# Kernel optimization log

Measured on AMD Instinct MI355X. Metric: run time of the kernel, lower is better.

Reference implementation:

```python
import jax, jax.numpy as jnp
import numpy as np

B, S, D, H = 8, 1024, 512, 12
HS = D // H  # 42 (head_size; 12*42 = 504 concat width, as in the original)


def setup_inputs() -> dict:
    key = jax.random.key(0)
    ks = jax.random.split(key, 12)
    sd = 0.02
    return {
        "embedded_patches": jax.random.normal(ks[0], (B, S, D), dtype=jnp.float32),
        # stacked per-head projections (12 independent Linear(D, HS, bias=False))
        "wk": jax.random.normal(ks[1], (H, D, HS), dtype=jnp.float32) * sd,
        "wq": jax.random.normal(ks[2], (H, D, HS), dtype=jnp.float32) * sd,
        "wv": jax.random.normal(ks[3], (H, D, HS), dtype=jnp.float32) * sd,
        "w_proj": jax.random.normal(ks[4], (H * HS, D), dtype=jnp.float32) * sd,  # [504, 512]
        "b_proj": jnp.zeros((D,), dtype=jnp.float32),
        # shared LayerNorm (same params used for both norms, as in the original)
        "gamma": jnp.ones((D,), dtype=jnp.float32),
        "beta": jnp.zeros((D,), dtype=jnp.float32),
        "w1": jax.random.normal(ks[5], (D, 4 * D), dtype=jnp.float32) * sd,
        "b1": jnp.zeros((4 * D,), dtype=jnp.float32),
        "w2": jax.random.normal(ks[6], (4 * D, D), dtype=jnp.float32) * sd,
        "b2": jnp.zeros((D,), dtype=jnp.float32),
    }


def _layernorm(x, gamma, beta, eps=1e-5):
    mu = jnp.mean(x, axis=-1, keepdims=True)
    var = jnp.var(x, axis=-1, keepdims=True)
    return (x - mu) * jax.lax.rsqrt(var + eps) * gamma + beta


def reference(embedded_patches, wk, wq, wv, w_proj, b_proj, gamma, beta, w1, b1, w2, b2):
    x = embedded_patches
    n1 = _layernorm(x, gamma, beta)
    # per-head projections, vectorized over heads: [B,S,D] x [H,D,E] -> [B,H,S,E]
    q = jnp.einsum('bsd,hde->bhse', n1, wq)
    k = jnp.einsum('bsd,hde->bhse', n1, wk)
    v = jnp.einsum('bsd,hde->bhse', n1, wv)
    scale = HS ** -0.5
    wei = jax.nn.softmax(jnp.einsum('bhse,bhte->bhst', q, k) * scale, axis=-1)
    out = jnp.einsum('bhst,bhte->bhse', wei, v)        # [B,H,S,E]
    out = out.transpose(0, 2, 1, 3).reshape(B, S, H * HS)  # concat heads -> [B,S,504]
    attn = out @ w_proj + b_proj                       # [B,S,D]
    # original quirk: takes batch element 0 and broadcasts against residual
    first_added = attn[0] + x                          # [S,D] + [B,S,D] -> [B,S,D]
    n2 = _layernorm(first_added, gamma, beta)
    h = jax.nn.gelu(n2 @ w1 + b1, approximate=False)   # torch nn.GELU default = exact erf
    ff = h @ w2 + b2
    return ff + first_added
```

## Files before the change

kernel.cpp:

```cpp
#include <hip/hip_runtime.h>
#include <hip/hip_bf16.h>
#include <stdint.h>


typedef unsigned short u16;
typedef __attribute__((ext_vector_type(8))) short short8;
typedef __attribute__((ext_vector_type(4))) float f32x4;

__device__ __forceinline__ u16 f2bf(float f) {
  union { float f; unsigned u; } x; x.f = f;
  return (u16)((x.u + 0x7FFFu + ((x.u >> 16) & 1u)) >> 16);
}
__device__ __forceinline__ float bf2f(u16 u) {
  union { unsigned u; float f; } x; x.u = ((unsigned)u) << 16;
  return x.f;
}

__device__ __forceinline__ void gload_lds16(const u16* g, u16* l) {
  __builtin_amdgcn_global_load_lds(
      (__attribute__((address_space(1))) void*)g,
      (__attribute__((address_space(3))) void*)l, 16, 0, 0);
}

__device__ __forceinline__ float wred_sum(float v) {
#pragma unroll
  for (int off = 32; off > 0; off >>= 1) v += __shfl_xor(v, off, 64);
  return v;
}
__device__ __forceinline__ float wred_max(float v) {
#pragma unroll
  for (int off = 32; off > 0; off >>= 1) v = fmaxf(v, __shfl_xor(v, off, 64));
  return v;
}

__device__ __forceinline__ float gelu_fast(float t) {
  const float p = __builtin_fmaf(0.0356774081f, t * t, 0.7978845608f);
  return t / (1.0f + __expf(-2.0f * t * p));
}

#define MFMA16x16(a, b, c) __builtin_amdgcn_mfma_f32_16x16x32_bf16(a, b, c, 0, 0, 0)

enum { EP_BF16 = 0, EP_F32B = 2, EP_GELU = 3, EP_PVPART = 6, EP_ATOM = 7 };

template <int EP>
__launch_bounds__(256, 4)
__global__ void gemm2(const u16* __restrict__ A, int lda, long sAz,
                      const u16* __restrict__ Bt, int ldb, long sBz,
                      void* __restrict__ Cv, int ldc, long sCz,
                      int K, const float* __restrict__ bias,
                      const float* __restrict__ aux) {
  __shared__ u16 lA[2][128 * 32];
  __shared__ u16 lB[2][128 * 32];

  const int gx = gridDim.x, gy = gridDim.y;
  const int lin = blockIdx.x + gx * (blockIdx.y + gy * blockIdx.z);
  const int nwg = gx * gy * gridDim.z;
  const int wg = (lin & 7) * (nwg >> 3) + (lin >> 3);
  const int bx = wg % gx;
  const int tmp = wg / gx;
  const int by = tmp % gy;
  const int z = tmp / gy;

  const u16* Ab;
  const u16* Bb;
  if (EP == EP_PVPART) {
    Ab = A + (long)(z >> 2) * sAz + (z & 3) * 256;
    Bb = Bt + (long)(z >> 2) * sBz + (z & 3) * 256;
  } else {
    Ab = A + (long)z * sAz;
    Bb = Bt + (long)z * sBz;
  }
  const int m0 = bx * 128;
  const int n0 = by * 128;
  const int tid = threadIdx.x;
  const int w = tid >> 6;
  const int l = tid & 63;
  const int wr = w >> 1;
  const int wc = w & 1;
  const int NT = K >> 5;

  f32x4 acc[4][4];
#pragma unroll
  for (int i = 0; i < 4; ++i)
#pragma unroll
    for (int j = 0; j < 4; ++j) acc[i][j] = (f32x4){0.f, 0.f, 0.f, 0.f};

  const int srow = w * 32 + (l >> 2);
  const int sk = (l & 3) * 8;
  const u16* ga0 = Ab + (long)(m0 + srow) * lda + sk;
  const u16* ga1 = Ab + (long)(m0 + srow + 16) * lda + sk;
  const u16* gb0 = Bb + (long)(n0 + srow) * ldb + sk;
  const u16* gb1 = Bb + (long)(n0 + srow + 16) * ldb + sk;
  const int dOff = w * 1024;

  const int aoff = (wr * 64 + (l & 15)) * 32 + (l >> 4) * 8;
  const int boff = (wc * 64 + (l & 15)) * 32 + (l >> 4) * 8;

  gload_lds16(ga0, &lA[0][dOff]);
  gload_lds16(ga1, &lA[0][dOff + 512]);
  gload_lds16(gb0, &lB[0][dOff]);
  gload_lds16(gb1, &lB[0][dOff + 512]);
  __syncthreads();

  int buf = 0;
  for (int t = 0; t < NT; ++t) {
    short8 af[4], bfv[4];
#pragma unroll
    for (int mi = 0; mi < 4; ++mi)
      af[mi] = *(const short8*)&lA[buf][aoff + mi * 16 * 32];
#pragma unroll
    for (int ni = 0; ni < 4; ++ni)
      bfv[ni] = *(const short8*)&lB[buf][boff + ni * 16 * 32];
    if (t + 1 < NT) {
      const int k0 = (t + 1) * 32;
      const int nb = buf ^ 1;
      gload_lds16(ga0 + k0, &lA[nb][dOff]);
      gload_lds16(ga1 + k0, &lA[nb][dOff + 512]);
      gload_lds16(gb0 + k0, &lB[nb][dOff]);
      gload_lds16(gb1 + k0, &lB[nb][dOff + 512]);
    }
#pragma unroll
    for (int mi = 0; mi < 4; ++mi)
#pragma unroll
      for (int ni = 0; ni < 4; ++ni)
        acc[mi][ni] = MFMA16x16(af[mi], bfv[ni], acc[mi][ni]);
    __syncthreads();
    buf ^= 1;
  }

  const int rbase = m0 + wr * 64 + (l >> 4) * 4;
  const int cbase = n0 + wc * 64 + (l & 15);
#pragma unroll
  for (int mi = 0; mi < 4; ++mi) {
#pragma unroll
    for (int ni = 0; ni < 4; ++ni) {
#pragma unroll
      for (int j = 0; j < 4; ++j) {
        const int row = rbase + mi * 16 + j;
        const int col = cbase + ni * 16;
        const float v = acc[mi][ni][j];
        if (EP == EP_BF16) {
          ((u16*)Cv)[(long)z * sCz + (long)row * ldc + col] = f2bf(v);
        } else if (EP == EP_F32B) {
          ((float*)Cv)[(long)row * ldc + col] = v + bias[col];
        } else if (EP == EP_GELU) {
          ((u16*)Cv)[(long)row * ldc + col] = f2bf(gelu_fast(v + bias[col]));
        } else if (EP == EP_PVPART) {
          ((float*)Cv)[(long)z * sCz + (long)row * ldc + col] = v;
        } else {
          atomicAdd(&((float*)Cv)[(long)row * ldc + col], v);
        }
      }
    }
  }
}

__global__ void combine_pv_kernel(const float* __restrict__ part,
                                  const float* __restrict__ invl,
                                  u16* __restrict__ cat) {
  const int i = blockIdx.x * 256 + threadIdx.x;
  const int e = i % 42;
  const int rowh = i / 42;
  const int row = rowh & 1023;
  const int h = rowh >> 10;
  const long base = (long)(h * 4) * 131072 + row * 128 + e;
  float v = part[base] + part[base + 131072] + part[base + 2 * 131072] +
            part[base + 3 * 131072];
  cat[(long)row * 512 + h * 42 + e] = f2bf(v * invl[h * 1024 + row]);
}

__device__ __forceinline__ void transpose_body(const float* __restrict__ in,
                                               u16* __restrict__ out, int N,
                                               int Kin, int Kpad, int blk,
                                               int gx, int t, float* smem) {
  const int n0 = (blk % gx) * 64;
  const int k0 = (blk / gx) * 64;
  const int tc = t & 63;
  const int tr = t >> 6;
#pragma unroll
  for (int r = 0; r < 16; ++r) {
    const int kr = tr * 16 + r;
    const int kg = k0 + kr;
    smem[kr * 65 + tc] = (kg < Kin) ? in[(long)kg * N + n0 + tc] : 0.f;
  }
  __syncthreads();
  const int nr0 = t >> 4;
  const int kc = (t & 15) * 4;
#pragma unroll
  for (int p = 0; p < 4; ++p) {
    const int nr = nr0 + p * 16;
    ushort4 v;
    v.x = f2bf(smem[(kc + 0) * 65 + nr]);
    v.y = f2bf(smem[(kc + 1) * 65 + nr]);
    v.z = f2bf(smem[(kc + 2) * 65 + nr]);
    v.w = f2bf(smem[(kc + 3) * 65 + nr]);
    *(ushort4*)&out[(long)(n0 + nr) * Kpad + k0 + kc] = v;
  }
}

__global__ void prep_fused(const float* __restrict__ wq,
                           const float* __restrict__ wk,
                           const float* __restrict__ wv,
                           const float* __restrict__ w_proj,
                           const float* __restrict__ w1,
                           const float* __restrict__ w2,
                           const float* __restrict__ x,
                           const float* __restrict__ gamma,
                           const float* __restrict__ beta,
                           u16* __restrict__ BtQKV, u16* __restrict__ wvT,
                           u16* __restrict__ BtP, u16* __restrict__ Bt1,
                           u16* __restrict__ Bt2, u16* __restrict__ cat,
                           u16* __restrict__ n1, float scale) {
  __shared__ float smem[64 * 65];
  const int blk = blockIdx.x;
  const int t = threadIdx.x;
  if (blk < 3072) {
    const int i = blk * 256 + t;
    const int n = i >> 9, d = i & 511;
    const int pq = n / 768;
    const int h = (n % 768) >> 6;
    const int e = n & 63;
    float v = 0.f;
    if (e < 42) {
      v = (pq ? wk : wq)[((long)h * 512 + d) * 42 + e];
      if (!pq) v *= scale;
    }
    BtQKV[i] = f2bf(v);
  } else if (blk < 6144) {
    const int i = (blk - 3072) * 256 + t;
    const int r = i >> 9, d = i & 511;
    const int h = r >> 7, e = r & 127;
    wvT[i] = f2bf(e < 42 ? wv[((long)h * 512 + d) * 42 + e] : 0.f);
  } else if (blk < 6208) {
    transpose_body(w_proj, BtP, 512, 504, 512, blk - 6144, 8, t, smem);
  } else if (blk < 6464) {
    transpose_body(w1, Bt1, 2048, 512, 512, blk - 6208, 32, t, smem);
  } else if (blk < 6720) {
    transpose_body(w2, Bt2, 512, 2048, 2048, blk - 6464, 8, t, smem);
  } else if (blk < 8768) {
    cat[(blk - 6720) * 256 + t] = 0;
  } else {
    const int s = blk - 8768;
    const float* row = x + (long)s * 512;
    const float v0 = row[t];
    const float v1 = row[t + 256];
    float sum = wred_sum(v0 + v1);
    float sq = wred_sum(v0 * v0 + v1 * v1);
    if ((t & 63) == 0) { smem[t >> 6] = sum; smem[8 + (t >> 6)] = sq; }
    __syncthreads();
    sum = smem[0] + smem[1] + smem[2] + smem[3];
    sq = smem[8] + smem[9] + smem[10] + smem[11];
    const float mu = sum * (1.0f / 512.0f);
    const float rstd = rsqrtf(sq * (1.0f / 512.0f) - mu * mu + 1e-5f);
    n1[(long)s * 512 + t] = f2bf((v0 - mu) * rstd * gamma[t] + beta[t]);
    n1[(long)s * 512 + t + 256] =
        f2bf((v1 - mu) * rstd * gamma[t + 256] + beta[t + 256]);
  }
}

__global__ void ln2_kernel(const float* __restrict__ x,
                           const float* __restrict__ aproj,
                           const float* __restrict__ gamma,
                           const float* __restrict__ beta,
                           const float* __restrict__ b2,
                           float* __restrict__ fa, u16* __restrict__ n2,
                           float* __restrict__ outp) {
  __shared__ float red[16];
  const int r = blockIdx.x;
  const int t = threadIdx.x;
  const int s = r & 1023;
  const float* xr = x + (long)r * 512;
  const float* ar = aproj + (long)s * 512;
  const float v0 = xr[t] + ar[t];
  const float v1 = xr[t + 256] + ar[t + 256];
  fa[(long)r * 512 + t] = v0;
  fa[(long)r * 512 + t + 256] = v1;
  outp[(long)r * 512 + t] = v0 + b2[t];
  outp[(long)r * 512 + t + 256] = v1 + b2[t + 256];
  float sum = wred_sum(v0 + v1);
  float sq = wred_sum(v0 * v0 + v1 * v1);
  if ((t & 63) == 0) { red[t >> 6] = sum; red[8 + (t >> 6)] = sq; }
  __syncthreads();
  sum = red[0] + red[1] + red[2] + red[3];
  sq = red[8] + red[9] + red[10] + red[11];
  const float mu = sum * (1.0f / 512.0f);
  const float rstd = rsqrtf(sq * (1.0f / 512.0f) - mu * mu + 1e-5f);
  n2[(long)r * 512 + t] = f2bf((v0 - mu) * rstd * gamma[t] + beta[t]);
  n2[(long)r * 512 + t + 256] =
      f2bf((v1 - mu) * rstd * gamma[t + 256] + beta[t + 256]);
}

__global__ void softmax_kernel(u16* __restrict__ SP, float* __restrict__ invl) {
  __shared__ float red[16];
  const long row = blockIdx.x;
  u16* p = SP + row * 1024;
  const int t = threadIdx.x;
  uint2 u = ((const uint2*)p)[t];
  const float s0 = bf2f((u16)(u.x & 0xffff));
  const float s1 = bf2f((u16)(u.x >> 16));
  const float s2 = bf2f((u16)(u.y & 0xffff));
  const float s3 = bf2f((u16)(u.y >> 16));
  float m = wred_max(fmaxf(fmaxf(s0, s1), fmaxf(s2, s3)));
  if ((t & 63) == 0) red[t >> 6] = m;
  __syncthreads();
  m = fmaxf(fmaxf(red[0], red[1]), fmaxf(red[2], red[3]));
  const float e0 = __expf(s0 - m), e1 = __expf(s1 - m);
  const float e2 = __expf(s2 - m), e3 = __expf(s3 - m);
  float sum = wred_sum(e0 + e1 + e2 + e3);
  if ((t & 63) == 0) red[8 + (t >> 6)] = sum;
  __syncthreads();
  sum = red[8] + red[9] + red[10] + red[11];
  if (t == 0) invl[row] = 1.0f / sum;
  uint2 o;
  o.x = (unsigned)f2bf(e0) | ((unsigned)f2bf(e1) << 16);
  o.y = (unsigned)f2bf(e2) | ((unsigned)f2bf(e3) << 16);
  ((uint2*)p)[t] = o;
}

extern "C" void kernel_launch(void* const* d_in, const int* in_sizes, int n_in,
                              void* d_out, int out_size, void* d_ws,
                              size_t ws_size, hipStream_t stream) {
  const float* x = (const float*)d_in[0];
  const float* wk = (const float*)d_in[1];
  const float* wq = (const float*)d_in[2];
  const float* wv = (const float*)d_in[3];
  const float* w_proj = (const float*)d_in[4];
  const float* b_proj = (const float*)d_in[5];
  const float* gamma = (const float*)d_in[6];
  const float* beta = (const float*)d_in[7];
  const float* w1 = (const float*)d_in[8];
  const float* b1 = (const float*)d_in[9];
  const float* w2 = (const float*)d_in[10];
  const float* b2 = (const float*)d_in[11];

  char* base = (char*)d_ws;
  size_t off = 0;
  auto alloc = [&](size_t bytes) -> void* {
    void* p = base + off;
    off += (bytes + 255) & ~(size_t)255;
    return p;
  };
  u16* n1 = (u16*)alloc(1024L * 512 * 2);
  u16* qkvc = (u16*)alloc(1024L * 1536 * 2);
  u16* SP = (u16*)alloc(12L * 1024 * 1024 * 2);
  u16* wvT = (u16*)alloc(1536L * 512 * 2);
  u16* vt = (u16*)alloc(1536L * 1024 * 2);
  u16* cat = (u16*)alloc(1024L * 512 * 2);
  float* aproj = (float*)alloc(1024L * 512 * 4);
  float* fa = (float*)alloc(8192L * 512 * 4);
  u16* n2 = (u16*)alloc(8192L * 512 * 2);
  u16* hbuf = (u16*)alloc(8192L * 2048 * 2);
  u16* BtQKV = (u16*)alloc(1536L * 512 * 2);
  u16* BtP = (u16*)alloc(512L * 512 * 2);
  u16* Bt1 = (u16*)alloc(2048L * 512 * 2);
  u16* Bt2 = (u16*)alloc(512L * 2048 * 2);
  float* invl = (float*)alloc(12L * 1024 * 4);
  float* pvpart = (float*)alloc(48L * 1024 * 128 * 4);
  (void)ws_size; (void)in_sizes; (void)n_in; (void)out_size;

  const float scale = 0.15430334996209191f;

  prep_fused<<<9792, 256, 0, stream>>>(wq, wk, wv, w_proj, w1, w2, x, gamma,
                                       beta, BtQKV, wvT, BtP, Bt1, Bt2, cat,
                                       n1, scale);

  gemm2<EP_BF16><<<dim3(8, 12, 1), 256, 0, stream>>>(
      n1, 512, 0, BtQKV, 512, 0, qkvc, 1536, 0, 512, nullptr, nullptr);
  gemm2<EP_BF16><<<dim3(12, 8, 1), 256, 0, stream>>>(
      wvT, 512, 0, n1, 512, 0, vt, 1024, 0, 512, nullptr, nullptr);
  gemm2<EP_BF16><<<dim3(8, 8, 12), 256, 0, stream>>>(
      qkvc, 1536, 64, qkvc + 768, 1536, 64, SP, 1024, 1024L * 1024, 64,
      nullptr, nullptr);
  softmax_kernel<<<12288, 256, 0, stream>>>(SP, invl);
  gemm2<EP_PVPART><<<dim3(8, 1, 48), 256, 0, stream>>>(
      SP, 1024, 1024L * 1024, vt, 1024, 128L * 1024, pvpart, 128,
      1024L * 128, 256, nullptr, nullptr);
  combine_pv_kernel<<<2016, 256, 0, stream>>>(pvpart, invl, cat);
  gemm2<EP_F32B><<<dim3(8, 4, 1), 256, 0, stream>>>(
      cat, 512, 0, BtP, 512, 0, aproj, 512, 0, 512, b_proj, nullptr);
  ln2_kernel<<<8192, 256, 0, stream>>>(x, aproj, gamma, beta, b2, fa, n2,
                                       (float*)d_out);
  gemm2<EP_GELU><<<dim3(64, 16, 1), 256, 0, stream>>>(
      n2, 512, 0, Bt1, 512, 0, hbuf, 2048, 0, 512, b1, nullptr);
  gemm2<EP_ATOM><<<dim3(64, 4, 2), 256, 0, stream>>>(
      hbuf, 2048, 1024, Bt2, 2048, 1024, d_out, 512, 0, 1024, nullptr,
      nullptr);
}
```

Measured before the change: 177.0 us.

## Fuse attention QK, softmax and PV into a single flash-attention kernel

```diff
diff --git a/kernel.cpp b/kernel.cpp
--- a/kernel.cpp
+++ b/kernel.cpp
@@ -27,11 +27,6 @@
   for (int off = 32; off > 0; off >>= 1) v += __shfl_xor(v, off, 64);
   return v;
 }
-__device__ __forceinline__ float wred_max(float v) {
-#pragma unroll
-  for (int off = 32; off > 0; off >>= 1) v = fmaxf(v, __shfl_xor(v, off, 64));
-  return v;
-}
 
 __device__ __forceinline__ float gelu_fast(float t) {
   const float p = __builtin_fmaf(0.0356774081f, t * t, 0.7978845608f);
@@ -40,15 +35,14 @@
 
 #define MFMA16x16(a, b, c) __builtin_amdgcn_mfma_f32_16x16x32_bf16(a, b, c, 0, 0, 0)
 
-enum { EP_BF16 = 0, EP_F32B = 2, EP_GELU = 3, EP_PVPART = 6, EP_ATOM = 7 };
+enum { EP_BF16 = 0, EP_F32B = 2, EP_GELU = 3, EP_ATOM = 7 };
 
 template <int EP>
 __launch_bounds__(256, 4)
 __global__ void gemm2(const u16* __restrict__ A, int lda, long sAz,
                       const u16* __restrict__ Bt, int ldb, long sBz,
                       void* __restrict__ Cv, int ldc, long sCz,
-                      int K, const float* __restrict__ bias,
-                      const float* __restrict__ aux) {
+                      int K, const float* __restrict__ bias) {
   __shared__ u16 lA[2][128 * 32];
   __shared__ u16 lB[2][128 * 32];
 
@@ -61,15 +55,8 @@
   const int by = tmp % gy;
   const int z = tmp / gy;
 
-  const u16* Ab;
-  const u16* Bb;
-  if (EP == EP_PVPART) {
-    Ab = A + (long)(z >> 2) * sAz + (z & 3) * 256;
-    Bb = Bt + (long)(z >> 2) * sBz + (z & 3) * 256;
-  } else {
-    Ab = A + (long)z * sAz;
-    Bb = Bt + (long)z * sBz;
-  }
+  const u16* Ab = A + (long)z * sAz;
+  const u16* Bb = Bt + (long)z * sBz;
   const int m0 = bx * 128;
   const int n0 = by * 128;
   const int tid = threadIdx.x;
@@ -145,8 +132,6 @@
           ((float*)Cv)[(long)row * ldc + col] = v + bias[col];
         } else if (EP == EP_GELU) {
           ((u16*)Cv)[(long)row * ldc + col] = f2bf(gelu_fast(v + bias[col]));
-        } else if (EP == EP_PVPART) {
-          ((float*)Cv)[(long)z * sCz + (long)row * ldc + col] = v;
         } else {
           atomicAdd(&((float*)Cv)[(long)row * ldc + col], v);
         }
@@ -155,18 +140,133 @@
   }
 }
 
-__global__ void combine_pv_kernel(const float* __restrict__ part,
-                                  const float* __restrict__ invl,
-                                  u16* __restrict__ cat) {
-  const int i = blockIdx.x * 256 + threadIdx.x;
-  const int e = i % 42;
-  const int rowh = i / 42;
-  const int row = rowh & 1023;
-  const int h = rowh >> 10;
-  const long base = (long)(h * 4) * 131072 + row * 128 + e;
-  float v = part[base] + part[base + 131072] + part[base + 2 * 131072] +
-            part[base + 3 * 131072];
-  cat[(long)row * 512 + h * 42 + e] = f2bf(v * invl[h * 1024 + row]);
+__device__ __forceinline__ short8 frag_read(const u16* base, int row, int ks,
+                                            int l) {
+  const int g = (ks * 4 + (l >> 4)) ^ (l & 7);
+  return *(const short8*)&base[row * 64 + g * 8];
+}
+
+__launch_bounds__(256, 2)
+__global__ void flash_attn(const u16* __restrict__ qkvc,
+                           const u16* __restrict__ vt,
+                           u16* __restrict__ cat) {
+  __shared__ u16 lQ[64 * 64];
+  __shared__ u16 lK[2][64 * 64];
+  __shared__ u16 lV[2][64 * 64];
+  __shared__ u16 lP[4][16 * 64];
+  const int h = blockIdx.x;
+  const int q0 = blockIdx.y * 64;
+  const int tid = threadIdx.x;
+  const int w = tid >> 6;
+  const int l = tid & 63;
+  const int sg = ((l & 7) ^ (l >> 3)) * 8;
+  const int sr = w * 8 + (l >> 3);
+
+#define FA_STAGE(t_, b_)                                                    \
+  do {                                                                      \
+    const int kv_ = (t_) * 64;                                              \
+    gload_lds16(qkvc + (long)(kv_ + sr) * 1536 + 768 + h * 64 + sg,         \
+                lK[b_] + w * 8 * 64);                                       \
+    gload_lds16(qkvc + (long)(kv_ + 32 + sr) * 1536 + 768 + h * 64 + sg,    \
+                lK[b_] + (32 + w * 8) * 64);                                \
+    gload_lds16(vt + (long)(h * 128 + sr) * 1024 + kv_ + sg,                \
+                lV[b_] + w * 8 * 64);                                       \
+    gload_lds16(vt + (long)(h * 128 + 32 + sr) * 1024 + kv_ + sg,           \
+                lV[b_] + (32 + w * 8) * 64);                                \
+  } while (0)
+
+  gload_lds16(qkvc + (long)(q0 + sr) * 1536 + h * 64 + sg, lQ + w * 8 * 64);
+  gload_lds16(qkvc + (long)(q0 + 32 + sr) * 1536 + h * 64 + sg,
+              lQ + (32 + w * 8) * 64);
+  FA_STAGE(0, 0);
+  __syncthreads();
+
+  const short8 qf0 = frag_read(lQ, w * 16 + (l & 15), 0, l);
+  const short8 qf1 = frag_read(lQ, w * 16 + (l & 15), 1, l);
+
+  f32x4 accO[4];
+  float m_run[4], l_run[4];
+#pragma unroll
+  for (int i = 0; i < 4; ++i) {
+    accO[i] = (f32x4){0.f, 0.f, 0.f, 0.f};
+    m_run[i] = -3.0e38f;
+    l_run[i] = 0.f;
+  }
+
+  int buf = 0;
+  for (int t = 0; t < 16; ++t) {
+    if (t + 1 < 16) FA_STAGE(t + 1, buf ^ 1);
+    f32x4 s[4];
+#pragma unroll
+    for (int ni = 0; ni < 4; ++ni) {
+      const short8 kf0 = frag_read(lK[buf], ni * 16 + (l & 15), 0, l);
+      const short8 kf1 = frag_read(lK[buf], ni * 16 + (l & 15), 1, l);
+      s[ni] = MFMA16x16(qf0, kf0, ((f32x4){0.f, 0.f, 0.f, 0.f}));
+      s[ni] = MFMA16x16(qf1, kf1, s[ni]);
+    }
+#pragma unroll
+    for (int j = 0; j < 4; ++j) {
+      float mx = fmaxf(fmaxf(s[0][j], s[1][j]), fmaxf(s[2][j], s[3][j]));
+      mx = fmaxf(mx, __shfl_xor(mx, 1));
+      mx = fmaxf(mx, __shfl_xor(mx, 2));
+      mx = fmaxf(mx, __shfl_xor(mx, 4));
+      mx = fmaxf(mx, __shfl_xor(mx, 8));
+      const float mn = fmaxf(m_run[j], mx);
+      const float corr = __expf(m_run[j] - mn);
+      m_run[j] = mn;
+      float ps = 0.f;
+#pragma unroll
+      for (int ni = 0; ni < 4; ++ni) {
+        const float p = __expf(s[ni][j] - mn);
+        s[ni][j] = p;
+        ps += p;
+      }
+      ps += __shfl_xor(ps, 1);
+      ps += __shfl_xor(ps, 2);
+      ps += __shfl_xor(ps, 4);
+      ps += __shfl_xor(ps, 8);
+      l_run[j] = l_run[j] * corr + ps;
+#pragma unroll
+      for (int ne = 0; ne < 4; ++ne) accO[ne][j] *= corr;
+    }
+#pragma unroll
+    for (int ni = 0; ni < 4; ++ni) {
+#pragma unroll
+      for (int j = 0; j < 4; ++j) {
+        const int row = (l >> 4) * 4 + j;
+        const int col = ni * 16 + (l & 15);
+        const int boff = row * 128 + (((col >> 3) ^ (row & 7)) << 4) +
+                         (col & 7) * 2;
+        *(u16*)((char*)lP[w] + boff) = f2bf(s[ni][j]);
+      }
+    }
+    asm volatile("s_waitcnt lgkmcnt(0)" ::: "memory");
+    __builtin_amdgcn_sched_barrier(0);
+    const short8 pf0 = frag_read(lP[w], (l & 15), 0, l);
+    const short8 pf1 = frag_read(lP[w], (l & 15), 1, l);
+#pragma unroll
+    for (int ne = 0; ne < 4; ++ne) {
+      const short8 vf0 = frag_read(lV[buf], ne * 16 + (l & 15), 0, l);
+      const short8 vf1 = frag_read(lV[buf], ne * 16 + (l & 15), 1, l);
+      accO[ne] = MFMA16x16(pf0, vf0, accO[ne]);
+      accO[ne] = MFMA16x16(pf1, vf1, accO[ne]);
+    }
+    __syncthreads();
+    buf ^= 1;
+  }
+#undef FA_STAGE
+
+#pragma unroll
+  for (int j = 0; j < 4; ++j) {
+    const float inv = 1.0f / l_run[j];
+    const int row = q0 + w * 16 + (l >> 4) * 4 + j;
+#pragma unroll
+    for (int ne = 0; ne < 4; ++ne) {
+      const int e = ne * 16 + (l & 15);
+      if (e < 42)
+        cat[(long)row * 512 + h * 42 + e] = f2bf(accO[ne][j] * inv);
+    }
+  }
 }
 
 __device__ __forceinline__ void transpose_body(const float* __restrict__ in,
@@ -196,6 +296,12 @@
     v.w = f2bf(smem[(kc + 3) * 65 + nr]);
     *(ushort4*)&out[(long)(n0 + nr) * Kpad + k0 + kc] = v;
   }
+}
+
+__device__ __forceinline__ float wredsum_lane(float v) {
+#pragma unroll
+  for (int off = 32; off > 0; off >>= 1) v += __shfl_xor(v, off, 64);
+  return v;
 }
 
 __global__ void prep_fused(const float* __restrict__ wq,
@@ -244,8 +350,8 @@
     const float* row = x + (long)s * 512;
     const float v0 = row[t];
     const float v1 = row[t + 256];
-    float sum = wred_sum(v0 + v1);
-    float sq = wred_sum(v0 * v0 + v1 * v1);
+    float sum = wredsum_lane(v0 + v1);
+    float sq = wredsum_lane(v0 * v0 + v1 * v1);
     if ((t & 63) == 0) { smem[t >> 6] = sum; smem[8 + (t >> 6)] = sq; }
     __syncthreads();
     sum = smem[0] + smem[1] + smem[2] + smem[3];
@@ -263,8 +369,7 @@
                            const float* __restrict__ gamma,
                            const float* __restrict__ beta,
                            const float* __restrict__ b2,
-                           float* __restrict__ fa, u16* __restrict__ n2,
-                           float* __restrict__ outp) {
+                           u16* __restrict__ n2, float* __restrict__ outp) {
   __shared__ float red[16];
   const int r = blockIdx.x;
   const int t = threadIdx.x;
@@ -273,8 +378,6 @@
   const float* ar = aproj + (long)s * 512;
   const float v0 = xr[t] + ar[t];
   const float v1 = xr[t + 256] + ar[t + 256];
-  fa[(long)r * 512 + t] = v0;
-  fa[(long)r * 512 + t + 256] = v1;
   outp[(long)r * 512 + t] = v0 + b2[t];
   outp[(long)r * 512 + t + 256] = v1 + b2[t + 256];
   float sum = wred_sum(v0 + v1);
@@ -288,33 +391,6 @@
   n2[(long)r * 512 + t] = f2bf((v0 - mu) * rstd * gamma[t] + beta[t]);
   n2[(long)r * 512 + t + 256] =
       f2bf((v1 - mu) * rstd * gamma[t + 256] + beta[t + 256]);
-}
-
-__global__ void softmax_kernel(u16* __restrict__ SP, float* __restrict__ invl) {
-  __shared__ float red[16];
-  const long row = blockIdx.x;
-  u16* p = SP + row * 1024;
-  const int t = threadIdx.x;
-  uint2 u = ((const uint2*)p)[t];
-  const float s0 = bf2f((u16)(u.x & 0xffff));
-  const float s1 = bf2f((u16)(u.x >> 16));
-  const float s2 = bf2f((u16)(u.y & 0xffff));
-  const float s3 = bf2f((u16)(u.y >> 16));
-  float m = wred_max(fmaxf(fmaxf(s0, s1), fmaxf(s2, s3)));
-  if ((t & 63) == 0) red[t >> 6] = m;
-  __syncthreads();
-  m = fmaxf(fmaxf(red[0], red[1]), fmaxf(red[2], red[3]));
-  const float e0 = __expf(s0 - m), e1 = __expf(s1 - m);
-  const float e2 = __expf(s2 - m), e3 = __expf(s3 - m);
-  float sum = wred_sum(e0 + e1 + e2 + e3);
-  if ((t & 63) == 0) red[8 + (t >> 6)] = sum;
-  __syncthreads();
-  sum = red[8] + red[9] + red[10] + red[11];
-  if (t == 0) invl[row] = 1.0f / sum;
-  uint2 o;
-  o.x = (unsigned)f2bf(e0) | ((unsigned)f2bf(e1) << 16);
-  o.y = (unsigned)f2bf(e2) | ((unsigned)f2bf(e3) << 16);
-  ((uint2*)p)[t] = o;
 }
 
 extern "C" void kernel_launch(void* const* d_in, const int* in_sizes, int n_in,
@@ -342,20 +418,16 @@
   };
   u16* n1 = (u16*)alloc(1024L * 512 * 2);
   u16* qkvc = (u16*)alloc(1024L * 1536 * 2);
-  u16* SP = (u16*)alloc(12L * 1024 * 1024 * 2);
   u16* wvT = (u16*)alloc(1536L * 512 * 2);
   u16* vt = (u16*)alloc(1536L * 1024 * 2);
   u16* cat = (u16*)alloc(1024L * 512 * 2);
   float* aproj = (float*)alloc(1024L * 512 * 4);
-  float* fa = (float*)alloc(8192L * 512 * 4);
   u16* n2 = (u16*)alloc(8192L * 512 * 2);
   u16* hbuf = (u16*)alloc(8192L * 2048 * 2);
   u16* BtQKV = (u16*)alloc(1536L * 512 * 2);
   u16* BtP = (u16*)alloc(512L * 512 * 2);
   u16* Bt1 = (u16*)alloc(2048L * 512 * 2);
   u16* Bt2 = (u16*)alloc(512L * 2048 * 2);
-  float* invl = (float*)alloc(12L * 1024 * 4);
-  float* pvpart = (float*)alloc(48L * 1024 * 128 * 4);
   (void)ws_size; (void)in_sizes; (void)n_in; (void)out_size;
 
   const float scale = 0.15430334996209191f;
@@ -365,24 +437,16 @@
                                        n1, scale);
 
   gemm2<EP_BF16><<<dim3(8, 12, 1), 256, 0, stream>>>(
-      n1, 512, 0, BtQKV, 512, 0, qkvc, 1536, 0, 512, nullptr, nullptr);
+      n1, 512, 0, BtQKV, 512, 0, qkvc, 1536, 0, 512, nullptr);
   gemm2<EP_BF16><<<dim3(12, 8, 1), 256, 0, stream>>>(
-      wvT, 512, 0, n1, 512, 0, vt, 1024, 0, 512, nullptr, nullptr);
-  gemm2<EP_BF16><<<dim3(8, 8, 12), 256, 0, stream>>>(
-      qkvc, 1536, 64, qkvc + 768, 1536, 64, SP, 1024, 1024L * 1024, 64,
-      nullptr, nullptr);
-  softmax_kernel<<<12288, 256, 0, stream>>>(SP, invl);
-  gemm2<EP_PVPART><<<dim3(8, 1, 48), 256, 0, stream>>>(
-      SP, 1024, 1024L * 1024, vt, 1024, 128L * 1024, pvpart, 128,
-      1024L * 128, 256, nullptr, nullptr);
-  combine_pv_kernel<<<2016, 256, 0, stream>>>(pvpart, invl, cat);
+      wvT, 512, 0, n1, 512, 0, vt, 1024, 0, 512, nullptr);
+  flash_attn<<<dim3(12, 16), 256, 0, stream>>>(qkvc, vt, cat);
   gemm2<EP_F32B><<<dim3(8, 4, 1), 256, 0, stream>>>(
-      cat, 512, 0, BtP, 512, 0, aproj, 512, 0, 512, b_proj, nullptr);
-  ln2_kernel<<<8192, 256, 0, stream>>>(x, aproj, gamma, beta, b2, fa, n2,
+      cat, 512, 0, BtP, 512, 0, aproj, 512, 0, 512, b_proj);
+  ln2_kernel<<<8192, 256, 0, stream>>>(x, aproj, gamma, beta, b2, n2,
                                        (float*)d_out);
   gemm2<EP_GELU><<<dim3(64, 16, 1), 256, 0, stream>>>(
-      n2, 512, 0, Bt1, 512, 0, hbuf, 2048, 0, 512, b1, nullptr);
+      n2, 512, 0, Bt1, 512, 0, hbuf, 2048, 0, 512, b1);
   gemm2<EP_ATOM><<<dim3(64, 4, 2), 256, 0, stream>>>(
-      hbuf, 2048, 1024, Bt2, 2048, 1024, d_out, 512, 0, 1024, nullptr,
-      nullptr);
-}
+      hbuf, 2048, 1024, Bt2, 2048, 1024, d_out, 512, 0, 1024, nullptr);
+}
```

After: 165.2 us. -6.7%, faster.
